# Kernel tuning notes

Hardware: AMD Instinct MI355X
Metric: run time of the kernel (lower is better)

Reference implementation:

```python
import jax, jax.numpy as jnp
import numpy as np

NUM_HEADS = 16
REF_CLUSTER = 0
TOP_RATIO = 0.3        # adaptive_sparsity(layer_idx=0) = min_sparsity
FRAME_SUBSAMPLE = 0.7  # frame_subsample_ratio in the torch code


def setup_inputs() -> dict:
    key = jax.random.key(0)
    k0, k1, k2 = jax.random.split(key, 3)
    B, S, P, C = 1, 32, 512, 1024
    N = S * P
    K, Fc = 4, 8  # K clusters of Fc frames each
    x = jax.random.normal(k0, (B, N, C), dtype=jnp.float32)
    W_qkv = jax.random.normal(k1, (C, 3 * C), dtype=jnp.float32) * (C ** -0.5)
    b_qkv = jnp.zeros((3 * C,), jnp.float32)
    W_proj = jax.random.normal(k2, (C, C), dtype=jnp.float32) * (C ** -0.5)
    b_proj = jnp.zeros((C,), jnp.float32)
    clusters = jnp.arange(S, dtype=jnp.int32).reshape(K, Fc)  # disjoint frame clusters
    keyframes = clusters[:, 0]  # one keyframe per cluster
    return {"x": x, "W_qkv": W_qkv, "b_qkv": b_qkv, "W_proj": W_proj,
            "b_proj": b_proj, "clusters": clusters, "keyframes": keyframes}


def _attn(q, k, v, scale):
    # flash_attn_func math: softmax(q k^T / sqrt(D)) v
    logits = jnp.einsum('bhqd,bhkd->bhqk', q, k) * scale
    return jnp.einsum('bhqk,bhkd->bhqd', jax.nn.softmax(logits, axis=-1), v)


def reference(x, W_qkv, b_qkv, W_proj, b_proj, clusters, keyframes):
    B, N, C = x.shape
    H = NUM_HEADS
    D = C // H
    K, Fc = clusters.shape
    S = K * Fc
    P = N // S
    scale = D ** -0.5

    # qkv projection -> q,k,v each [B, H, S, P, D]
    qkv = (x @ W_qkv + b_qkv).reshape(B, N, 3, H, D)
    q, k, v = [jnp.transpose(qkv[:, :, i], (0, 2, 1, 3)).reshape(B, H, S, P, D)
               for i in range(3)]

    # coarse: keyframe prototype scores -> topk patches per cluster
    q_proto = q[:, :, keyframes]  # [B,H,K,P,D]
    k_proto = k[:, :, keyframes]
    attn_score = jnp.mean(jnp.max(jnp.sum(k_proto * q_proto, axis=-1), axis=1), axis=0)  # [K,P]
    tk = max(1, int(P * TOP_RATIO))
    _, patch_idx = jax.lax.top_k(attn_score, tk)  # [K, tk]

    n_sub = max(1, int(Fc * FRAME_SUBSAMPLE))
    out_frames = jnp.zeros((B, H, S, P, D), x.dtype)
    for ci in range(K):
        frame_ids = clusters[ci]
        q_local = q[:, :, frame_ids].reshape(B, H, Fc * P, D)
        k_parts, v_parts = [], []
        for nc in range(K):
            # deterministic stand-in for torch.randperm frame subsampling
            sampled = clusters[nc] if nc in (REF_CLUSTER, ci) else clusters[nc][:n_sub]
            pidx = patch_idx[nc]
            k_parts.append(k[:, :, sampled][:, :, :, pidx].reshape(B, H, -1, D))
            v_parts.append(v[:, :, sampled][:, :, :, pidx].reshape(B, H, -1, D))
        k_local = jnp.concatenate(k_parts, axis=2)
        v_local = jnp.concatenate(v_parts, axis=2)
        out_local = _attn(q_local, k_local, v_local, scale).reshape(B, H, Fc, P, D)
        out_frames = out_frames.at[:, :, frame_ids].add(out_local)

    out = jnp.transpose(out_frames.reshape(B, H, N, D), (0, 2, 1, 3)).reshape(B, N, C)
    return out @ W_proj + b_proj
```

## Files before the change

kernel.cpp:

```cpp
#include <hip/hip_runtime.h>
#include <hip/hip_bf16.h>
#include <hip/hip_fp16.h>

#define DEVINL __device__ __forceinline__

using short8 = __attribute__((ext_vector_type(8))) short;
using half8  = __attribute__((ext_vector_type(8))) _Float16;
using half2v = __attribute__((ext_vector_type(2))) _Float16;
using f32x4  = __attribute__((ext_vector_type(4))) float;
using uint4v = __attribute__((ext_vector_type(4))) unsigned;

static constexpr int N_TOK = 16384;
static constexpr int NH    = 16;
static constexpr int HD    = 64;
static constexpr int KCL   = 4;
static constexpr int TK    = 153;
static constexpr int LMAX  = 4096;

typedef __attribute__((address_space(1))) unsigned GU32;
typedef __attribute__((address_space(3))) unsigned LU32;

DEVINL void gload16(const void* g, void* l) {
    __builtin_amdgcn_global_load_lds((const GU32*)g, (LU32*)l, 16, 0, 0);
}

#if __has_builtin(__builtin_amdgcn_exp2f)
#define EXP2(x) __builtin_amdgcn_exp2f(x)
#else
#define EXP2(x) exp2f(x)
#endif

DEVINL void plswap32(unsigned& a, unsigned& b) {
#if __has_builtin(__builtin_amdgcn_permlane32_swap)
    auto r = __builtin_amdgcn_permlane32_swap(a, b, false, false);
    a = r[0]; b = r[1];
#else
    asm volatile("v_permlane32_swap_b32 %0, %1" : "+v"(a), "+v"(b));
#endif
}
DEVINL void plswap16(unsigned& a, unsigned& b) {
#if __has_builtin(__builtin_amdgcn_permlane16_swap)
    auto r = __builtin_amdgcn_permlane16_swap(a, b, false, false);
    a = r[0]; b = r[1];
#else
    asm volatile("v_permlane16_swap_b32 %0, %1" : "+v"(a), "+v"(b));
#endif
}

DEVINL unsigned short f2bf(float f) {
    unsigned u = __float_as_uint(f);
    unsigned r = u + 0x7FFFu + ((u >> 16) & 1u);
    return (unsigned short)(r >> 16);
}
DEVINL float bf2f(unsigned short h) { return __uint_as_float(((unsigned)h) << 16); }

__global__ void prep_w_kernel(const float* __restrict__ W, short* __restrict__ Btp,
                              int ncols) {
    int total = ncols * 2048;
    for (int o = blockIdx.x * blockDim.x + threadIdx.x; o < total;
         o += gridDim.x * blockDim.x) {
        int j = o >> 11, k = o & 2047, kk = k & 1023;
        float w = W[(size_t)kk * ncols + j];
        unsigned short hv = f2bf(w);
        unsigned short r = (k < 1024) ? hv : f2bf(w - bf2f(hv));
        Btp[o] = (short)r;
    }
}

template <int EPI>
__global__ __launch_bounds__(256)
void gemm_split(const float* __restrict__ xf32, const _Float16* __restrict__ xf16,
                const short* __restrict__ Btp, const float* __restrict__ bias,
                int nbn, _Float16* __restrict__ qkvh, float* __restrict__ protoF,
                float* __restrict__ outF) {
    __shared__ short Ah[2][4096], Al[2][4096], Bh[2][4096], Bl[2][4096];
    int tid = threadIdx.x, wid = tid >> 6;
    int lane = tid & 63, lr = lane & 15, lg = lane >> 4;
    int bid = blockIdx.x;
    int nb = bid % nbn, mb = bid / nbn;
    int m0 = mb * 128, n0 = nb * 128;
    int wm = wid >> 1, wn = wid & 1;

    f32x4 acc[4][4];
#pragma unroll
    for (int i = 0; i < 4; i++)
#pragma unroll
        for (int j = 0; j < 4; j++)
#pragma unroll
            for (int r = 0; r < 4; r++) acc[i][j][r] = 0.f;

    int brow = tid >> 2, bcc = tid & 3;
    int arow = tid >> 2, acol = tid & 3;

    float fva[2][8];

    auto issueB = [&](int kt, int buf) {
        int kk0 = kt * 32;
        gload16(Btp + (size_t)(n0 + brow) * 2048 + kk0 + bcc * 8, &Bh[buf][wid * 512]);
        gload16(Btp + (size_t)(n0 + 64 + brow) * 2048 + kk0 + bcc * 8, &Bh[buf][2048 + wid * 512]);
        gload16(Btp + (size_t)(n0 + brow) * 2048 + 1024 + kk0 + bcc * 8, &Bl[buf][wid * 512]);
        gload16(Btp + (size_t)(n0 + 64 + brow) * 2048 + 1024 + kk0 + bcc * 8, &Bl[buf][2048 + wid * 512]);
    };
    auto loadA = [&](int kt) {
        int kk0 = kt * 32;
#pragma unroll
        for (int p = 0; p < 2; p++) {
            int row = m0 + p * 64 + arow;
            int k = kk0 + acol * 8;
            if constexpr (EPI == 0) {
                const float* src = xf32 + (size_t)row * 1024 + k;
                f32x4 t0 = *(const f32x4*)src;
                f32x4 t1 = *(const f32x4*)(src + 4);
#pragma unroll
                for (int j = 0; j < 4; j++) { fva[p][j] = t0[j]; fva[p][4 + j] = t1[j]; }
            } else {
                const _Float16* src = xf16 + (size_t)(k >> 6) * ((size_t)N_TOK * HD)
                                      + (size_t)row * 64 + (k & 63);
                half8 g = *(const half8*)src;
#pragma unroll
                for (int j = 0; j < 8; j++) fva[p][j] = (float)g[j];
            }
        }
    };
    auto writeA = [&](int buf) {
#pragma unroll
        for (int p = 0; p < 2; p++) {
            short8 h8, l8;
#pragma unroll
            for (int j = 0; j < 8; j++) {
                float v = fva[p][j];
                unsigned short hv = f2bf(v);
                h8[j] = (short)hv;
                l8[j] = (short)f2bf(v - bf2f(hv));
            }
            *(short8*)(&Ah[buf][p * 2048 + tid * 8]) = h8;
            *(short8*)(&Al[buf][p * 2048 + tid * 8]) = l8;
        }
    };

    issueB(0, 0);
    loadA(0);
    writeA(0);
    __syncthreads();

    for (int kt = 0; kt < 32; ++kt) {
        int cur = kt & 1, nxt = cur ^ 1;
        if (kt + 1 < 32) {
            issueB(kt + 1, nxt);
            loadA(kt + 1);
        }

        short8 ah[4], al[4], bh[4], bl[4];
#pragma unroll
        for (int mi = 0; mi < 4; mi++) {
            int ro = (wm * 64 + mi * 16 + lr) * 32 + lg * 8;
            ah[mi] = *(const short8*)(&Ah[cur][ro]);
            al[mi] = *(const short8*)(&Al[cur][ro]);
        }
#pragma unroll
        for (int ni = 0; ni < 4; ni++) {
            int ro = (wn * 64 + ni * 16 + lr) * 32 + lg * 8;
            bh[ni] = *(const short8*)(&Bh[cur][ro]);
            bl[ni] = *(const short8*)(&Bl[cur][ro]);
        }
#pragma unroll
        for (int mi = 0; mi < 4; mi++)
#pragma unroll
            for (int ni = 0; ni < 4; ni++) {
                acc[mi][ni] = __builtin_amdgcn_mfma_f32_16x16x32_bf16(ah[mi], bh[ni], acc[mi][ni], 0, 0, 0);
                acc[mi][ni] = __builtin_amdgcn_mfma_f32_16x16x32_bf16(al[mi], bh[ni], acc[mi][ni], 0, 0, 0);
                acc[mi][ni] = __builtin_amdgcn_mfma_f32_16x16x32_bf16(ah[mi], bl[ni], acc[mi][ni], 0, 0, 0);
            }

        if (kt + 1 < 32) writeA(nxt);
        __syncthreads();
    }

#pragma unroll
    for (int mi = 0; mi < 4; mi++) {
#pragma unroll
        for (int ni = 0; ni < 4; ni++) {
            int col = n0 + wn * 64 + ni * 16 + lr;
            float bv = bias[col];
#pragma unroll
            for (int r = 0; r < 4; r++) {
                int rowm = m0 + wm * 64 + mi * 16 + lg * 4 + r;
                float val = acc[mi][ni][r] + bv;
                if constexpr (EPI == 0) {
                    int i3 = col >> 10, h = (col >> 6) & 15, d = col & 63;
                    qkvh[(((size_t)i3 * NH + h) * N_TOK + rowm) * HD + d] = (_Float16)val;
                    int s = rowm >> 9;
                    if (i3 < 2 && (s & 7) == 0) {
                        int kf = s >> 3, p = rowm & 511;
                        protoF[(((size_t)i3 * KCL + kf) * 512 + p) * (NH * HD) + h * HD + d] = val;
                    }
                } else {
                    outF[(size_t)rowm * 1024 + col] = val;
                }
            }
        }
    }
}

__global__ __launch_bounds__(256)
void score_kernel(const float* __restrict__ protoF, float* __restrict__ scores) {
    int tid = threadIdx.x, lane = tid & 63;
    int pos = blockIdx.x * 4 + (tid >> 6);
    int kc = pos >> 9, p = pos & 511;
    const float* qp = protoF + ((size_t)kc * 512 + p) * (NH * HD);
    const float* kp = protoF + ((size_t)(KCL + kc) * 512 + p) * (NH * HD);
    int hh = lane >> 2, dp = (lane & 3) * 16;
    float sum = 0.f;
#pragma unroll
    for (int i = 0; i < 16; i++) sum += qp[hh * 64 + dp + i] * kp[hh * 64 + dp + i];
    sum += __shfl_xor(sum, 1, 64);
    sum += __shfl_xor(sum, 2, 64);
    float v = ((lane & 3) == 0) ? sum : -1e30f;
    for (int m = 4; m < 64; m <<= 1) v = fmaxf(v, __shfl_xor(v, m, 64));
    if (lane == 0) scores[pos] = v;
}

__global__ __launch_bounds__(64)
void topk_kernel(const float* __restrict__ scores, int* __restrict__ pidx) {
    int ci = blockIdx.x, lane = threadIdx.x;
    float v[8];
#pragma unroll
    for (int m = 0; m < 8; m++) v[m] = scores[ci * 512 + lane * 8 + m];
    for (int i = 0; i < TK; i++) {
        float best = -1e30f; int bj = 0;
#pragma unroll
        for (int m = 0; m < 8; m++) if (v[m] > best) { best = v[m]; bj = m; }
        int bidx = lane * 8 + bj;
        for (int mk = 1; mk < 64; mk <<= 1) {
            float ov = __shfl_xor(best, mk, 64);
            int   oi = __shfl_xor(bidx, mk, 64);
            if (ov > best || (ov == best && oi < bidx)) { best = ov; bidx = oi; }
        }
        bool own = ((bidx >> 3) == lane);
        int sel = bidx - lane * 8;
#pragma unroll
        for (int m = 0; m < 8; m++) if (own && m == sel) v[m] = -1e30f;
        if (lane == 0) pidx[ci * TK + i] = bidx;
    }
}

__global__ __launch_bounds__(256)
void nlist_kernel(const int* __restrict__ pidx, int* __restrict__ nlist) {
    int ci = blockIdx.x;
    int L = TK * (ci == 0 ? 23 : 26);
    for (int pos = threadIdx.x; pos < L; pos += 256) {
        int seg = pos / TK, j = pos - seg * TK;
        int nc = 0, fi = 0, acc = 0;
        for (int c = 0; c < 4; c++) {
            int cnt = (c == 0 || c == ci) ? 8 : 5;
            if (seg >= acc && seg < acc + cnt) { nc = c; fi = seg - acc; }
            acc += cnt;
        }
        nlist[ci * LMAX + pos] = (nc * 8 + fi) * 512 + pidx[nc * TK + j];
    }
}

__global__ __launch_bounds__(256)
void gatherv_kernel(const _Float16* __restrict__ qkvh, const int* __restrict__ nlist,
                    _Float16* __restrict__ vT) {
    __shared__ _Float16 vrow[64 * 80];
    int bid = blockIdx.x;
    int t64 = bid & 63, h = (bid >> 6) & 15, ci = bid >> 10;
    int L = TK * (ci == 0 ? 23 : 26);
    const _Float16* vsrc = qkvh + (size_t)2 * NH * N_TOK * HD + (size_t)h * N_TOK * HD;
    int tid = threadIdx.x;
#pragma unroll
    for (int rep = 0; rep < 2; rep++) {
        int c = rep * 256 + tid; int row = c >> 3, cc = c & 7;
        int kvg = t64 * 64 + row;
        half8 val;
#pragma unroll
        for (int j = 0; j < 8; j++) val[j] = (_Float16)0.f;
        if (kvg < L) {
            int n = nlist[ci * LMAX + kvg];
            val = *(const half8*)(vsrc + (size_t)n * HD + cc * 8);
        }
        *(half8*)(vrow + row * 80 + cc * 8) = val;
    }
    __syncthreads();
#pragma unroll
    for (int rep = 0; rep < 2; rep++) {
        int c = rep * 256 + tid; int d = c >> 3, kvc = c & 7;
        half8 ov;
#pragma unroll
        for (int j = 0; j < 8; j++) ov[j] = vrow[(kvc * 8 + j) * 80 + d];
        *(half8*)(vT + ((size_t)(ci * 16 + h) * 64 + d) * LMAX + t64 * 64 + kvc * 8) = ov;
    }
}

__global__ __launch_bounds__(512)
void attn_kernel(const _Float16* __restrict__ qkvh, const _Float16* __restrict__ vT,
                 const int* __restrict__ nlist, _Float16* __restrict__ outh) {
    __shared__ _Float16 kt[2][4096];
    __shared__ _Float16 vt[2][4096];
    int bid = blockIdx.x;
    int qb = bid & 15, h = (bid >> 4) & 15, ci = bid >> 8;
    int tid = threadIdx.x, wid = tid >> 6, lane = tid & 63;
    int lr = lane & 15, lg = lane >> 4;
    int L = TK * (ci == 0 ? 23 : 26);
    int nt = (L + 63) >> 6;

    const _Float16* qh = qkvh;
    const _Float16* kh = qkvh + (size_t)NH * N_TOK * HD;
    int qrow0 = ci * 4096 + qb * 256 + wid * 32;

    const _Float16 qsc = (_Float16)0.180336880f;
    half8 qf[2][2];
#pragma unroll
    for (int g = 0; g < 2; g++)
#pragma unroll
        for (int ks = 0; ks < 2; ks++) {
            qf[g][ks] = *(const half8*)(qh + ((size_t)h * N_TOK + qrow0 + g * 16 + lr) * HD
                                        + ks * 32 + lg * 8);
#pragma unroll
            for (int j = 0; j < 8; j++) qf[g][ks][j] *= qsc;
        }
    half8 ones;
#pragma unroll
    for (int j = 0; j < 8; j++) ones[j] = (_Float16)1.f;

    f32x4 o[2][4], lacc[2];
    float mrun[2];
#pragma unroll
    for (int g = 0; g < 2; g++) {
#pragma unroll
        for (int nd = 0; nd < 4; nd++)
#pragma unroll
            for (int r = 0; r < 4; r++) o[g][nd][r] = 0.f;
#pragma unroll
        for (int r = 0; r < 4; r++) lacc[g][r] = 0.f;
        mrun[g] = -1e30f;
    }

    int krow = tid >> 3, kcc = tid & 7;
    int swz = (kcc ^ (krow & 7)) * 8;
    const int* nl = nlist + ci * LMAX;
    const _Float16* vTb = vT + ((size_t)(ci * 16 + h) * 64 + krow) * LMAX;
    size_t khbase = (size_t)h * N_TOK;

    int n_cur = (krow < L) ? nl[krow] : 0;
    gload16(kh + (khbase + n_cur) * HD + swz, &kt[0][wid * 512]);
    gload16(vTb + swz, &vt[0][wid * 512]);
    int kvg1 = 64 + krow;
    int n_nxt = (kvg1 < L) ? nl[kvg1] : 0;

    for (int t = 0; t < nt; t++) {
        asm volatile("s_waitcnt vmcnt(0)" ::: "memory");
        __builtin_amdgcn_sched_barrier(0);
        __builtin_amdgcn_s_barrier();
        __builtin_amdgcn_sched_barrier(0);

        if (t + 1 < nt) {
            gload16(kh + (khbase + n_nxt) * HD + swz, &kt[(t + 1) & 1][wid * 512]);
            gload16(vTb + (t + 1) * 64 + swz, &vt[(t + 1) & 1][wid * 512]);
            int kvg2 = (t + 2) * 64 + krow;
            n_nxt = (kvg2 < L) ? nl[kvg2] : 0;
        }

        const _Float16* ktb = kt[t & 1];
        const _Float16* vtb = vt[t & 1];

        f32x4 s[2][4];
#pragma unroll
        for (int g = 0; g < 2; g++)
#pragma unroll
            for (int ni = 0; ni < 4; ni++)
#pragma unroll
                for (int r = 0; r < 4; r++) s[g][ni][r] = 0.f;
#pragma unroll
        for (int ni = 0; ni < 4; ni++)
#pragma unroll
            for (int ks = 0; ks < 2; ks++) {
                int row = ni * 16 + lr;
                half8 kb = *(const half8*)(ktb + row * 64 + (((ks * 4 + lg) ^ (row & 7)) * 8));
                s[0][ni] = __builtin_amdgcn_mfma_f32_16x16x32_f16(kb, qf[0][ks], s[0][ni], 0, 0, 0);
                s[1][ni] = __builtin_amdgcn_mfma_f32_16x16x32_f16(kb, qf[1][ks], s[1][ni], 0, 0, 0);
            }
        if (t == nt - 1) {
#pragma unroll
            for (int ni = 0; ni < 4; ni++) {
                int kvv = t * 64 + ni * 16 + lg * 4;
#pragma unroll
                for (int r = 0; r < 4; r++)
                    if (kvv + r >= L) { s[0][ni][r] = -1e30f; s[1][ni][r] = -1e30f; }
            }
        }

        float mloc[2];
#pragma unroll
        for (int g = 0; g < 2; g++) {
            float m0 = fmaxf(fmaxf(s[g][0][0], s[g][0][1]), fmaxf(s[g][0][2], s[g][0][3]));
            float m1 = fmaxf(fmaxf(s[g][1][0], s[g][1][1]), fmaxf(s[g][1][2], s[g][1][3]));
            float m2 = fmaxf(fmaxf(s[g][2][0], s[g][2][1]), fmaxf(s[g][2][2], s[g][2][3]));
            float m3 = fmaxf(fmaxf(s[g][3][0], s[g][3][1]), fmaxf(s[g][3][2], s[g][3][3]));
            mloc[g] = fmaxf(fmaxf(m0, m1), fmaxf(m2, m3));
        }
        bool ok = (mloc[0] <= mrun[0] + 8.f) && (mloc[1] <= mrun[1] + 8.f);
        if (!__all(ok)) {
#pragma unroll
            for (int g = 0; g < 2; g++) {
                float mt = mloc[g];
                mt = fmaxf(mt, __shfl_xor(mt, 16, 64));
                mt = fmaxf(mt, __shfl_xor(mt, 32, 64));
                float mn = fmaxf(mrun[g], mt);
                float corr = EXP2(mrun[g] - mn);
                mrun[g] = mn;
#pragma unroll
                for (int r = 0; r < 4; r++) lacc[g][r] *= corr;
#pragma unroll
                for (int nd = 0; nd < 4; nd++)
#pragma unroll
                    for (int r = 0; r < 4; r++) o[g][nd][r] *= corr;
            }
        }

        half8 pf[2][2];
#pragma unroll
        for (int g = 0; g < 2; g++) {
            float p[4][4];
#pragma unroll
            for (int ni = 0; ni < 4; ni++)
#pragma unroll
                for (int r = 0; r < 4; r++) p[ni][r] = EXP2(s[g][ni][r] - mrun[g]);
            unsigned c[4][2];
#pragma unroll
            for (int ni = 0; ni < 4; ni++) {
                c[ni][0] = __builtin_bit_cast(unsigned, __builtin_amdgcn_cvt_pkrtz(p[ni][0], p[ni][1]));
                c[ni][1] = __builtin_bit_cast(unsigned, __builtin_amdgcn_cvt_pkrtz(p[ni][2], p[ni][3]));
            }
#pragma unroll
            for (int ksv = 0; ksv < 2; ksv++) {
                unsigned a0 = c[2 * ksv][0], a1 = c[2 * ksv][1];
                unsigned b0 = c[2 * ksv + 1][0], b1 = c[2 * ksv + 1][1];
                plswap32(a0, b0); plswap32(a1, b1);
                plswap16(a0, b0); plswap16(a1, b1);
                uint4v w = {a0, a1, b0, b1};
                pf[g][ksv] = __builtin_bit_cast(half8, w);
            }
        }

#pragma unroll
        for (int nd = 0; nd < 4; nd++)
#pragma unroll
            for (int ksv = 0; ksv < 2; ksv++) {
                int row = nd * 16 + lr;
                half8 vb = *(const half8*)(vtb + row * 64 + (((ksv * 4 + lg) ^ (row & 7)) * 8));
                o[0][nd] = __builtin_amdgcn_mfma_f32_16x16x32_f16(vb, pf[0][ksv], o[0][nd], 0, 0, 0);
                o[1][nd] = __builtin_amdgcn_mfma_f32_16x16x32_f16(vb, pf[1][ksv], o[1][nd], 0, 0, 0);
            }
#pragma unroll
        for (int g = 0; g < 2; g++)
#pragma unroll
            for (int ksv = 0; ksv < 2; ksv++)
                lacc[g] = __builtin_amdgcn_mfma_f32_16x16x32_f16(ones, pf[g][ksv], lacc[g], 0, 0, 0);
    }

#pragma unroll
    for (int g = 0; g < 2; g++) {
        float inv = 1.f / lacc[g][0];
        int qg = qrow0 + g * 16 + lr;
        unsigned* dst = (unsigned*)(outh + (size_t)h * N_TOK * HD + (size_t)qg * 64);
#pragma unroll
        for (int nd = 0; nd < 4; nd++)
#pragma unroll
            for (int rp = 0; rp < 2; rp++) {
                half2v hv;
                hv[0] = (_Float16)(o[g][nd][2 * rp] * inv);
                hv[1] = (_Float16)(o[g][nd][2 * rp + 1] * inv);
                dst[(nd * 16 + lg * 4) / 2 + rp] = __builtin_bit_cast(unsigned, hv);
            }
    }
}

extern "C" void kernel_launch(void* const* d_in, const int* in_sizes, int n_in,
                              void* d_out, int out_size, void* d_ws, size_t ws_size,
                              hipStream_t stream) {
    (void)in_sizes; (void)n_in; (void)out_size;
    const float* x     = (const float*)d_in[0];
    const float* Wqkv  = (const float*)d_in[1];
    const float* bqkv  = (const float*)d_in[2];
    const float* Wproj = (const float*)d_in[3];
    const float* bproj = (const float*)d_in[4];

    char* ws = (char*)d_ws;
    size_t off = 0;
    auto alloc = [&](size_t bytes) -> void* {
        void* p = ws + off; off += (bytes + 255) & ~(size_t)255; return p;
    };
    short*    Btp1   = (short*)alloc((size_t)3072 * 2048 * 2);
    short*    Btp2   = (short*)alloc((size_t)1024 * 2048 * 2);
    _Float16* qkvh   = (_Float16*)alloc((size_t)3 * NH * N_TOK * HD * 2);
    void*     R1     = alloc((size_t)KCL * NH * HD * LMAX * 2);
    float*    scores = (float*)alloc((size_t)KCL * 512 * 4);
    int*      pidx   = (int*)alloc((size_t)KCL * TK * 4);
    int*      nlist  = (int*)alloc((size_t)KCL * LMAX * 4);
    if (ws_size < off) return;

    float*    protoF = (float*)R1;
    _Float16* vT     = (_Float16*)R1;
    _Float16* vout   = qkvh + (size_t)2 * NH * N_TOK * HD;

    prep_w_kernel<<<2048, 256, 0, stream>>>(Wqkv, Btp1, 3072);
    prep_w_kernel<<<1024, 256, 0, stream>>>(Wproj, Btp2, 1024);

    gemm_split<0><<<128 * 24, 256, 0, stream>>>(x, nullptr, Btp1, bqkv, 24,
                                                qkvh, protoF, nullptr);

    score_kernel<<<512, 256, 0, stream>>>(protoF, scores);
    topk_kernel<<<4, 64, 0, stream>>>(scores, pidx);
    nlist_kernel<<<4, 256, 0, stream>>>(pidx, nlist);
    gatherv_kernel<<<4096, 256, 0, stream>>>(qkvh, nlist, vT);

    attn_kernel<<<1024, 512, 0, stream>>>(qkvh, vT, nlist, vout);

    gemm_split<1><<<128 * 8, 256, 0, stream>>>(nullptr, vout, Btp2, bproj, 8,
                                               nullptr, nullptr, (float*)d_out);
}
```

Baseline: 1.114 ms.

## Pre-split GEMM A operands into bf16 hi/lo and load via async LDS

Adds a prep kernel that converts x into bf16 hi/lo halves, and makes the attention kernel write its output directly in the same split layout. A new GEMM variant then streams both A and B through global_load_lds with an XOR-swizzled LDS layout, so the per-tile float conversion inside the GEMM main loop goes away. The new GEMM is single-buffered, with a sync after the loads, so it gives up the old load/compute overlap. It also needs an extra 64MB workspace buffer and falls back to the old path if the workspace is too small.

```diff
diff --git a/kernel.cpp b/kernel.cpp
--- a/kernel.cpp
+++ b/kernel.cpp
@@ -4,6 +4,7 @@
 
 #define DEVINL __device__ __forceinline__
 
+using short4v = __attribute__((ext_vector_type(4))) short;
 using short8 = __attribute__((ext_vector_type(8))) short;
 using half8  = __attribute__((ext_vector_type(8))) _Float16;
 using half2v = __attribute__((ext_vector_type(2))) _Float16;
@@ -67,13 +68,30 @@
     }
 }
 
+__global__ void prep_x_kernel(const float* __restrict__ x, short* __restrict__ A) {
+    for (size_t ii = (size_t)blockIdx.x * blockDim.x + threadIdx.x;
+         ii < (size_t)N_TOK * 256; ii += (size_t)gridDim.x * blockDim.x) {
+        size_t row = ii >> 8; int c4 = (int)(ii & 255) * 4;
+        f32x4 v = *(const f32x4*)(x + row * 1024 + c4);
+        short4v h, l;
+#pragma unroll
+        for (int j = 0; j < 4; j++) {
+            unsigned short hv = f2bf(v[j]);
+            h[j] = (short)hv;
+            l[j] = (short)f2bf(v[j] - bf2f(hv));
+        }
+        *(short4v*)(A + row * 2048 + c4) = h;
+        *(short4v*)(A + row * 2048 + 1024 + c4) = l;
+    }
+}
+
 template <int EPI>
 __global__ __launch_bounds__(256)
-void gemm_split(const float* __restrict__ xf32, const _Float16* __restrict__ xf16,
-                const short* __restrict__ Btp, const float* __restrict__ bias,
-                int nbn, _Float16* __restrict__ qkvh, float* __restrict__ protoF,
-                float* __restrict__ outF) {
-    __shared__ short Ah[2][4096], Al[2][4096], Bh[2][4096], Bl[2][4096];
+void gemm_as(const short* __restrict__ Atp, const short* __restrict__ Btp,
+             const float* __restrict__ bias, int nbn,
+             _Float16* __restrict__ qkvh, float* __restrict__ protoF,
+             float* __restrict__ outF) {
+    __shared__ short Ah[4096], Al[4096], Bh[4096], Bl[4096];
     int tid = threadIdx.x, wid = tid >> 6;
     int lane = tid & 63, lr = lane & 15, lg = lane >> 4;
     int bid = blockIdx.x;
@@ -89,79 +107,37 @@
 #pragma unroll
             for (int r = 0; r < 4; r++) acc[i][j][r] = 0.f;
 
-    int brow = tid >> 2, bcc = tid & 3;
-    int arow = tid >> 2, acol = tid & 3;
-
-    float fva[2][8];
-
-    auto issueB = [&](int kt, int buf) {
+    int r0 = tid >> 2, cc = tid & 3;
+    int sw0 = (cc ^ ((r0 >> 1) & 3)) * 8;
+    const short* Ab = Atp + (size_t)m0 * 2048;
+    const short* Bb = Btp + (size_t)n0 * 2048;
+
+    for (int kt = 0; kt < 32; ++kt) {
         int kk0 = kt * 32;
-        gload16(Btp + (size_t)(n0 + brow) * 2048 + kk0 + bcc * 8, &Bh[buf][wid * 512]);
-        gload16(Btp + (size_t)(n0 + 64 + brow) * 2048 + kk0 + bcc * 8, &Bh[buf][2048 + wid * 512]);
-        gload16(Btp + (size_t)(n0 + brow) * 2048 + 1024 + kk0 + bcc * 8, &Bl[buf][wid * 512]);
-        gload16(Btp + (size_t)(n0 + 64 + brow) * 2048 + 1024 + kk0 + bcc * 8, &Bl[buf][2048 + wid * 512]);
-    };
-    auto loadA = [&](int kt) {
-        int kk0 = kt * 32;
-#pragma unroll
-        for (int p = 0; p < 2; p++) {
-            int row = m0 + p * 64 + arow;
-            int k = kk0 + acol * 8;
-            if constexpr (EPI == 0) {
-                const float* src = xf32 + (size_t)row * 1024 + k;
-                f32x4 t0 = *(const f32x4*)src;
-                f32x4 t1 = *(const f32x4*)(src + 4);
-#pragma unroll
-                for (int j = 0; j < 4; j++) { fva[p][j] = t0[j]; fva[p][4 + j] = t1[j]; }
-            } else {
-                const _Float16* src = xf16 + (size_t)(k >> 6) * ((size_t)N_TOK * HD)
-                                      + (size_t)row * 64 + (k & 63);
-                half8 g = *(const half8*)src;
-#pragma unroll
-                for (int j = 0; j < 8; j++) fva[p][j] = (float)g[j];
-            }
-        }
-    };
-    auto writeA = [&](int buf) {
-#pragma unroll
-        for (int p = 0; p < 2; p++) {
-            short8 h8, l8;
-#pragma unroll
-            for (int j = 0; j < 8; j++) {
-                float v = fva[p][j];
-                unsigned short hv = f2bf(v);
-                h8[j] = (short)hv;
-                l8[j] = (short)f2bf(v - bf2f(hv));
-            }
-            *(short8*)(&Ah[buf][p * 2048 + tid * 8]) = h8;
-            *(short8*)(&Al[buf][p * 2048 + tid * 8]) = l8;
-        }
-    };
-
-    issueB(0, 0);
-    loadA(0);
-    writeA(0);
-    __syncthreads();
-
-    for (int kt = 0; kt < 32; ++kt) {
-        int cur = kt & 1, nxt = cur ^ 1;
-        if (kt + 1 < 32) {
-            issueB(kt + 1, nxt);
-            loadA(kt + 1);
-        }
+        gload16(Ab + (size_t)r0 * 2048 + kk0 + sw0, Ah + wid * 512);
+        gload16(Ab + (size_t)(64 + r0) * 2048 + kk0 + sw0, Ah + 2048 + wid * 512);
+        gload16(Ab + (size_t)r0 * 2048 + 1024 + kk0 + sw0, Al + wid * 512);
+        gload16(Ab + (size_t)(64 + r0) * 2048 + 1024 + kk0 + sw0, Al + 2048 + wid * 512);
+        gload16(Bb + (size_t)r0 * 2048 + kk0 + sw0, Bh + wid * 512);
+        gload16(Bb + (size_t)(64 + r0) * 2048 + kk0 + sw0, Bh + 2048 + wid * 512);
+        gload16(Bb + (size_t)r0 * 2048 + 1024 + kk0 + sw0, Bl + wid * 512);
+        gload16(Bb + (size_t)(64 + r0) * 2048 + 1024 + kk0 + sw0, Bl + 2048 + wid * 512);
+        __syncthreads();
 
         short8 ah[4], al[4], bh[4], bl[4];
 #pragma unroll
         for (int mi = 0; mi < 4; mi++) {
-            int ro = (wm * 64 + mi * 16 + lr) * 32 + lg * 8;
-            ah[mi] = *(const short8*)(&Ah[cur][ro]);
-            al[mi] = *(const short8*)(&Al[cur][ro]);
+            int ro = wm * 64 + mi * 16 + lr;
+            int off = ro * 32 + (lg ^ ((ro >> 1) & 3)) * 8;
+            ah[mi] = *(const short8*)(&Ah[off]);
+            al[mi] = *(const short8*)(&Al[off]);
         }
 #pragma unroll
         for (int ni = 0; ni < 4; ni++) {
-            int ro = (wn * 64 + ni * 16 + lr) * 32 + lg * 8;
-            bh[ni] = *(const short8*)(&Bh[cur][ro]);
-            bl[ni] = *(const short8*)(&Bl[cur][ro]);
+            int ro = wn * 64 + ni * 16 + lr;
+            int off = ro * 32 + (lg ^ ((ro >> 1) & 3)) * 8;
+            bh[ni] = *(const short8*)(&Bh[off]);
+            bl[ni] = *(const short8*)(&Bl[off]);
         }
 #pragma unroll
         for (int mi = 0; mi < 4; mi++)
@@ -171,8 +147,6 @@
                 acc[mi][ni] = __builtin_amdgcn_mfma_f32_16x16x32_bf16(al[mi], bh[ni], acc[mi][ni], 0, 0, 0);
                 acc[mi][ni] = __builtin_amdgcn_mfma_f32_16x16x32_bf16(ah[mi], bl[ni], acc[mi][ni], 0, 0, 0);
             }
-
-        if (kt + 1 < 32) writeA(nxt);
         __syncthreads();
     }
 
@@ -202,6 +176,137 @@
     }
 }
 
+template <int EPI>
+__global__ __launch_bounds__(256)
+void gemm_split(const float* __restrict__ xf32, const _Float16* __restrict__ xf16,
+                const short* __restrict__ Btp, const float* __restrict__ bias,
+                int nbn, _Float16* __restrict__ qkvh, float* __restrict__ protoF,
+                float* __restrict__ outF) {
+    __shared__ short Ah[2][4096], Al[2][4096], Bh[2][4096], Bl[2][4096];
+    int tid = threadIdx.x, wid = tid >> 6;
+    int lane = tid & 63, lr = lane & 15, lg = lane >> 4;
+    int bid = blockIdx.x;
+    int nb = bid % nbn, mb = bid / nbn;
+    int m0 = mb * 128, n0 = nb * 128;
+    int wm = wid >> 1, wn = wid & 1;
+
+    f32x4 acc[4][4];
+#pragma unroll
+    for (int i = 0; i < 4; i++)
+#pragma unroll
+        for (int j = 0; j < 4; j++)
+#pragma unroll
+            for (int r = 0; r < 4; r++) acc[i][j][r] = 0.f;
+
+    int brow = tid >> 2, bcc = tid & 3;
+    int arow = tid >> 2, acol = tid & 3;
+    float fva[2][8];
+
+    auto issueB = [&](int kt, int buf) {
+        int kk0 = kt * 32;
+        gload16(Btp + (size_t)(n0 + brow) * 2048 + kk0 + bcc * 8, &Bh[buf][wid * 512]);
+        gload16(Btp + (size_t)(n0 + 64 + brow) * 2048 + kk0 + bcc * 8, &Bh[buf][2048 + wid * 512]);
+        gload16(Btp + (size_t)(n0 + brow) * 2048 + 1024 + kk0 + bcc * 8, &Bl[buf][wid * 512]);
+        gload16(Btp + (size_t)(n0 + 64 + brow) * 2048 + 1024 + kk0 + bcc * 8, &Bl[buf][2048 + wid * 512]);
+    };
+    auto loadA = [&](int kt) {
+        int kk0 = kt * 32;
+#pragma unroll
+        for (int p = 0; p < 2; p++) {
+            int row = m0 + p * 64 + arow;
+            int k = kk0 + acol * 8;
+            if constexpr (EPI == 0) {
+                const float* src = xf32 + (size_t)row * 1024 + k;
+                f32x4 t0 = *(const f32x4*)src;
+                f32x4 t1 = *(const f32x4*)(src + 4);
+#pragma unroll
+                for (int j = 0; j < 4; j++) { fva[p][j] = t0[j]; fva[p][4 + j] = t1[j]; }
+            } else {
+                const _Float16* src = xf16 + (size_t)(k >> 6) * ((size_t)N_TOK * HD)
+                                      + (size_t)row * 64 + (k & 63);
+                half8 g = *(const half8*)src;
+#pragma unroll
+                for (int j = 0; j < 8; j++) fva[p][j] = (float)g[j];
+            }
+        }
+    };
+    auto writeA = [&](int buf) {
+#pragma unroll
+        for (int p = 0; p < 2; p++) {
+            short8 h8, l8;
+#pragma unroll
+            for (int j = 0; j < 8; j++) {
+                float v = fva[p][j];
+                unsigned short hv = f2bf(v);
+                h8[j] = (short)hv;
+                l8[j] = (short)f2bf(v - bf2f(hv));
+            }
+            *(short8*)(&Ah[buf][p * 2048 + tid * 8]) = h8;
+            *(short8*)(&Al[buf][p * 2048 + tid * 8]) = l8;
+        }
+    };
+
+    issueB(0, 0);
+    loadA(0);
+    writeA(0);
+    __syncthreads();
+
+    for (int kt = 0; kt < 32; ++kt) {
+        int cur = kt & 1, nxt = cur ^ 1;
+        if (kt + 1 < 32) { issueB(kt + 1, nxt); loadA(kt + 1); }
+
+        short8 ah[4], al[4], bh[4], bl[4];
+#pragma unroll
+        for (int mi = 0; mi < 4; mi++) {
+            int ro = (wm * 64 + mi * 16 + lr) * 32 + lg * 8;
+            ah[mi] = *(const short8*)(&Ah[cur][ro]);
+            al[mi] = *(const short8*)(&Al[cur][ro]);
+        }
+#pragma unroll
+        for (int ni = 0; ni < 4; ni++) {
+            int ro = (wn * 64 + ni * 16 + lr) * 32 + lg * 8;
+            bh[ni] = *(const short8*)(&Bh[cur][ro]);
+            bl[ni] = *(const short8*)(&Bl[cur][ro]);
+        }
+#pragma unroll
+        for (int mi = 0; mi < 4; mi++)
+#pragma unroll
+            for (int ni = 0; ni < 4; ni++) {
+                acc[mi][ni] = __builtin_amdgcn_mfma_f32_16x16x32_bf16(ah[mi], bh[ni], acc[mi][ni], 0, 0, 0);
+                acc[mi][ni] = __builtin_amdgcn_mfma_f32_16x16x32_bf16(al[mi], bh[ni], acc[mi][ni], 0, 0, 0);
+                acc[mi][ni] = __builtin_amdgcn_mfma_f32_16x16x32_bf16(ah[mi], bl[ni], acc[mi][ni], 0, 0, 0);
+            }
+
+        if (kt + 1 < 32) writeA(nxt);
+        __syncthreads();
+    }
+
+#pragma unroll
+    for (int mi = 0; mi < 4; mi++) {
+#pragma unroll
+        for (int ni = 0; ni < 4; ni++) {
+            int col = n0 + wn * 64 + ni * 16 + lr;
+            float bv = bias[col];
+#pragma unroll
+            for (int r = 0; r < 4; r++) {
+                int rowm = m0 + wm * 64 + mi * 16 + lg * 4 + r;
+                float val = acc[mi][ni][r] + bv;
+                if constexpr (EPI == 0) {
+                    int i3 = col >> 10, h = (col >> 6) & 15, d = col & 63;
+                    qkvh[(((size_t)i3 * NH + h) * N_TOK + rowm) * HD + d] = (_Float16)val;
+                    int s = rowm >> 9;
+                    if (i3 < 2 && (s & 7) == 0) {
+                        int kf = s >> 3, p = rowm & 511;
+                        protoF[(((size_t)i3 * KCL + kf) * 512 + p) * (NH * HD) + h * HD + d] = val;
+                    }
+                } else {
+                    outF[(size_t)rowm * 1024 + col] = val;
+                }
+            }
+        }
+    }
+}
+
 __global__ __launch_bounds__(256)
 void score_kernel(const float* __restrict__ protoF, float* __restrict__ scores) {
     int tid = threadIdx.x, lane = tid & 63;
@@ -293,9 +398,11 @@
     }
 }
 
+template <int OUT>
 __global__ __launch_bounds__(512)
 void attn_kernel(const _Float16* __restrict__ qkvh, const _Float16* __restrict__ vT,
-                 const int* __restrict__ nlist, _Float16* __restrict__ outh) {
+                 const int* __restrict__ nlist, _Float16* __restrict__ outh,
+                 short* __restrict__ A2) {
     __shared__ _Float16 kt[2][4096];
     __shared__ _Float16 vt[2][4096];
     int bid = blockIdx.x;
@@ -464,16 +571,33 @@
     for (int g = 0; g < 2; g++) {
         float inv = 1.f / lacc[g][0];
         int qg = qrow0 + g * 16 + lr;
-        unsigned* dst = (unsigned*)(outh + (size_t)h * N_TOK * HD + (size_t)qg * 64);
-#pragma unroll
-        for (int nd = 0; nd < 4; nd++)
-#pragma unroll
-            for (int rp = 0; rp < 2; rp++) {
-                half2v hv;
-                hv[0] = (_Float16)(o[g][nd][2 * rp] * inv);
-                hv[1] = (_Float16)(o[g][nd][2 * rp + 1] * inv);
-                dst[(nd * 16 + lg * 4) / 2 + rp] = __builtin_bit_cast(unsigned, hv);
-            }
+        if constexpr (OUT == 0) {
+            unsigned* dst = (unsigned*)(outh + (size_t)h * N_TOK * HD + (size_t)qg * 64);
+#pragma unroll
+            for (int nd = 0; nd < 4; nd++)
+#pragma unroll
+                for (int rp = 0; rp < 2; rp++) {
+                    half2v hv;
+                    hv[0] = (_Float16)(o[g][nd][2 * rp] * inv);
+                    hv[1] = (_Float16)(o[g][nd][2 * rp + 1] * inv);
+                    dst[(nd * 16 + lg * 4) / 2 + rp] = __builtin_bit_cast(unsigned, hv);
+                }
+        } else {
+            short* dst = A2 + (size_t)qg * 2048;
+#pragma unroll
+            for (int nd = 0; nd < 4; nd++)
+#pragma unroll
+                for (int rp = 0; rp < 2; rp++) {
+                    float v0 = o[g][nd][2 * rp] * inv;
+                    float v1 = o[g][nd][2 * rp + 1] * inv;
+                    unsigned h0 = f2bf(v0), h1 = f2bf(v1);
+                    unsigned l0 = f2bf(v0 - bf2f((unsigned short)h0));
+                    unsigned l1 = f2bf(v1 - bf2f((unsigned short)h1));
+                    int c = h * 64 + nd * 16 + lg * 4 + 2 * rp;
+                    *(unsigned*)(dst + c)        = h0 | (h1 << 16);
+                    *(unsigned*)(dst + 1024 + c) = l0 | (l1 << 16);
+                }
+        }
     }
 }
 
@@ -499,7 +623,10 @@
     float*    scores = (float*)alloc((size_t)KCL * 512 * 4);
     int*      pidx   = (int*)alloc((size_t)KCL * TK * 4);
     int*      nlist  = (int*)alloc((size_t)KCL * LMAX * 4);
-    if (ws_size < off) return;
+    size_t off_min = off;
+    short*    A12    = (short*)alloc((size_t)N_TOK * 2048 * 2);
+    if (ws_size < off_min) return;
+    bool big = (ws_size >= off);
 
     float*    protoF = (float*)R1;
     _Float16* vT     = (_Float16*)R1;
@@ -508,16 +635,27 @@
     prep_w_kernel<<<2048, 256, 0, stream>>>(Wqkv, Btp1, 3072);
     prep_w_kernel<<<1024, 256, 0, stream>>>(Wproj, Btp2, 1024);
 
-    gemm_split<0><<<128 * 24, 256, 0, stream>>>(x, nullptr, Btp1, bqkv, 24,
-                                                qkvh, protoF, nullptr);
+    if (big) {
+        prep_x_kernel<<<2048, 256, 0, stream>>>(x, A12);
+        gemm_as<0><<<128 * 24, 256, 0, stream>>>(A12, Btp1, bqkv, 24,
+                                                 qkvh, protoF, nullptr);
+    } else {
+        gemm_split<0><<<128 * 24, 256, 0, stream>>>(x, nullptr, Btp1, bqkv, 24,
+                                                    qkvh, protoF, nullptr);
+    }
 
     score_kernel<<<512, 256, 0, stream>>>(protoF, scores);
     topk_kernel<<<4, 64, 0, stream>>>(scores, pidx);
     nlist_kernel<<<4, 256, 0, stream>>>(pidx, nlist);
     gatherv_kernel<<<4096, 256, 0, stream>>>(qkvh, nlist, vT);
 
-    attn_kernel<<<1024, 512, 0, stream>>>(qkvh, vT, nlist, vout);
-
-    gemm_split<1><<<128 * 8, 256, 0, stream>>>(nullptr, vout, Btp2, bproj, 8,
-                                               nullptr, nullptr, (float*)d_out);
-}
+    if (big) {
+        attn_kernel<1><<<1024, 512, 0, stream>>>(qkvh, vT, nlist, nullptr, A12);
+        gemm_as<1><<<128 * 8, 256, 0, stream>>>(A12, Btp2, bproj, 8,
+                                                nullptr, nullptr, (float*)d_out);
+    } else {
+        attn_kernel<0><<<1024, 512, 0, stream>>>(qkvh, vT, nlist, vout, nullptr);
+        gemm_split<1><<<128 * 8, 256, 0, stream>>>(nullptr, vout, Btp2, bproj, 8,
+                                                   nullptr, nullptr, (float*)d_out);
+    }
+}
```

Result: faster. 1.035 ms (-7.1%).
